# Performance work log

Measured on AMD Instinct MI355X. Metric: run time of the kernel, lower is better.

Reference implementation:

```python
import jax, jax.numpy as jnp
import numpy as np

NEG_INF = -1e6  # d2l masked_softmax fill value


def setup_inputs() -> dict:
    key = jax.random.key(0)
    ks = jax.random.split(key, 7)
    B, Q, K, D, H = 16, 64, 512, 256, 256
    querys = jax.random.normal(ks[0], (B, Q, D), dtype=jnp.float32)
    keys = jax.random.normal(ks[1], (B, K, D), dtype=jnp.float32)
    values = jax.random.normal(ks[2], (B, K, D), dtype=jnp.float32)
    valid_lens = jax.random.randint(ks[3], (B,), 1, K + 1)
    # learned parameters (Linear weights stored as (in, out) for x @ W)
    Wq = jax.random.normal(ks[4], (D, H), dtype=jnp.float32) / np.sqrt(D)
    Wk = jax.random.normal(ks[5], (D, H), dtype=jnp.float32) / np.sqrt(D)
    w_v = jax.random.normal(ks[6], (H,), dtype=jnp.float32) / np.sqrt(H)
    return {"querys": querys, "keys": keys, "values": values,
            "valid_lens": valid_lens, "Wq": Wq, "Wk": Wk, "w_v": w_v}


def reference(querys, keys, values, valid_lens, Wq, Wk, w_v):
    B, Q, _ = querys.shape
    K = keys.shape[1]
    q = querys @ Wq                      # (B, Q, H)
    k = keys @ Wk                        # (B, K, H)
    features = jnp.tanh(q[:, :, None, :] + k[:, None, :, :])   # (B, Q, K, H)
    scores = jnp.einsum('bqkh,h->bqk', features, w_v)           # (B, Q, K)
    # masked softmax over key axis: positions >= valid_len get -1e6
    mask = jnp.arange(K)[None, None, :] < valid_lens[:, None, None]  # (B,1,K)
    scores = jnp.where(mask, scores, NEG_INF)
    attn = jax.nn.softmax(scores, axis=-1)                       # (B, Q, K)
    return jnp.einsum('bqk,bkd->bqd', attn, values)              # (B, Q, D)
```

## Files before the change

### kernel.cpp

```cpp
#include <hip/hip_runtime.h>

#define BB 16
#define QQ 64
#define KK 512
#define DD 256
#define HH 256
#define KTILE 128
#define NZ 4
#define LDST 56

#define LOG2E2 2.88539008177792681f

typedef unsigned int uint;
typedef unsigned short ushort;
typedef __attribute__((ext_vector_type(8))) short bf16x8;
typedef __attribute__((ext_vector_type(8))) unsigned short ushort8;
typedef __attribute__((ext_vector_type(4))) float f32x4;

__device__ __forceinline__ float fast_exp2(float x) {
#if __has_builtin(__builtin_amdgcn_exp2f)
    return __builtin_amdgcn_exp2f(x);
#else
    return exp2f(x);
#endif
}

__device__ __forceinline__ ushort f32_to_bf16_rtne(float x) {
    uint u = __float_as_uint(x);
    u = (u + 0x7FFFu + ((u >> 16) & 1u)) >> 16;
    return (ushort)u;
}

__device__ __forceinline__ void cvt8(uint4 u, float4& a, float4& b) {
    a.x = __uint_as_float(u.x << 16); a.y = __uint_as_float(u.x & 0xFFFF0000u);
    a.z = __uint_as_float(u.y << 16); a.w = __uint_as_float(u.y & 0xFFFF0000u);
    b.x = __uint_as_float(u.z << 16); b.y = __uint_as_float(u.z & 0xFFFF0000u);
    b.z = __uint_as_float(u.w << 16); b.w = __uint_as_float(u.w & 0xFFFF0000u);
}

__global__ __launch_bounds__(256) void proj_both(
        const float* __restrict__ Xq, const float* __restrict__ Wq, float* __restrict__ Yq,
        const float* __restrict__ Xk, const float* __restrict__ Wk, ushort* __restrict__ Yk16,
        const int* __restrict__ valid_lens) {
    __shared__ ushort As[64 * LDST];
    __shared__ ushort Bt[64 * LDST];
    const int rt = blockIdx.x;
    const bool is_q = (rt < 16);
    const float* X; const float* W; int row0;
    if (is_q) { X = Xq; W = Wq; row0 = rt * 64; }
    else {
        X = Xk; W = Wk; row0 = (rt - 16) * 64;
        const int bb    = row0 >> 9;
        const int local = row0 & 511;
        if (local >= valid_lens[bb]) return;
    }
    const int col0 = blockIdx.y * 64;
    const int tid  = threadIdx.x;
    const int lane = tid & 63;
    const int w    = tid >> 6;

    f32x4 acc[4] = {{0.f,0.f,0.f,0.f}, {0.f,0.f,0.f,0.f},
                    {0.f,0.f,0.f,0.f}, {0.f,0.f,0.f,0.f}};

    const int ar = tid >> 2;
    const int ak = (tid & 3) * 8;
    const int bc = tid & 15;
    const int bk = tid >> 4;

    for (int k0 = 0; k0 < HH; k0 += 32) {
        {
            const float* xp = X + (size_t)(row0 + ar) * HH + k0 + ak;
            float4 x0 = *(const float4*)(xp);
            float4 x1 = *(const float4*)(xp + 4);
            ushort8 o;
            o[0] = f32_to_bf16_rtne(x0.x); o[1] = f32_to_bf16_rtne(x0.y);
            o[2] = f32_to_bf16_rtne(x0.z); o[3] = f32_to_bf16_rtne(x0.w);
            o[4] = f32_to_bf16_rtne(x1.x); o[5] = f32_to_bf16_rtne(x1.y);
            o[6] = f32_to_bf16_rtne(x1.z); o[7] = f32_to_bf16_rtne(x1.w);
            *(ushort8*)(&As[ar * LDST + ak]) = o;
        }
        {
            #pragma unroll
            for (int s = 0; s < 2; ++s) {
                float4 wv = *(const float4*)(W + (size_t)(k0 + bk + 16*s) * HH + col0 + bc*4);
                Bt[(bc*4 + 0) * LDST + bk + 16*s] = f32_to_bf16_rtne(wv.x);
                Bt[(bc*4 + 1) * LDST + bk + 16*s] = f32_to_bf16_rtne(wv.y);
                Bt[(bc*4 + 2) * LDST + bk + 16*s] = f32_to_bf16_rtne(wv.z);
                Bt[(bc*4 + 3) * LDST + bk + 16*s] = f32_to_bf16_rtne(wv.w);
            }
        }
        __syncthreads();

        const bf16x8 af = *(const bf16x8*)(&As[(w*16 + (lane & 15)) * LDST + (lane >> 4) * 8]);
        #pragma unroll
        for (int ct = 0; ct < 4; ++ct) {
            const bf16x8 bf = *(const bf16x8*)(&Bt[(ct*16 + (lane & 15)) * LDST + (lane >> 4) * 8]);
            acc[ct] = __builtin_amdgcn_mfma_f32_16x16x32_bf16(af, bf, acc[ct], 0, 0, 0);
        }
        __syncthreads();
    }

    const int orow = row0 + w*16 + (lane >> 4) * 4;
    const int ocol = col0 + (lane & 15);
    if (is_q) {
        #pragma unroll
        for (int ct = 0; ct < 4; ++ct)
            #pragma unroll
            for (int j = 0; j < 4; ++j)
                Yq[(size_t)(orow + j) * HH + ocol + ct*16] = acc[ct][j] * LOG2E2;
    } else {
        #pragma unroll
        for (int ct = 0; ct < 4; ++ct)
            #pragma unroll
            for (int j = 0; j < 4; ++j)
                Yk16[(size_t)(orow + j) * HH + ocol + ct*16] =
                    f32_to_bf16_rtne(acc[ct][j] * LOG2E2);
    }
}

__global__ __launch_bounds__(256) void fused_flash(
        const float* __restrict__ qf, const ushort* __restrict__ kf16,
        const float* __restrict__ w_v, const int* __restrict__ valid_lens,
        const float* __restrict__ values,
        float* __restrict__ pm, float* __restrict__ pl, float* __restrict__ po) {
    __shared__ float qls[8][16][20];
    __shared__ float sc[8][KTILE];
    __shared__ float pp[8][KTILE];
    __shared__ float red[4][8][DD];

    const int tid  = threadIdx.x;
    const int lane = tid & 63;
    const int w    = tid >> 6;
    const int hg   = lane & 15;
    const int ksub = lane >> 4;
    const int h0   = hg * 16;

    int TT = 0;
    #pragma unroll
    for (int i = 0; i < BB; ++i)
        TT += (valid_lens[i] + KTILE - 1) >> 7;

    const int xcd = blockIdx.x & 7;
    const int j   = blockIdx.x >> 3;
    const int tl  = xcd + 8 * (j >> 3);
    const int oct = j & 7;
    if (tl >= TT) return;
    const int q0 = oct * 8;

    int bb = 0, zz = 0, vlb = 1, acc = 0;
    #pragma unroll
    for (int i = 0; i < BB; ++i) {
        const int v   = valid_lens[i];
        const int nzi = (v + KTILE - 1) >> 7;
        const bool hit = (tl >= acc) && (tl < acc + nzi);
        if (hit) { bb = i; zz = tl - acc; vlb = v; }
        acc += nzi;
    }
    const int tile_lo = zz * KTILE;
    const int tile_hi = (tile_lo + KTILE < vlb) ? (tile_lo + KTILE) : vlb;

    float4 nw[4];
    float wvsum = 0.f;
    #pragma unroll
    for (int i = 0; i < 4; ++i) {
        float4 wv4 = *(const float4*)(w_v + h0 + i*4);
        wvsum += ((wv4.x + wv4.y) + (wv4.z + wv4.w));
        nw[i] = make_float4(-2.f*wv4.x, -2.f*wv4.y, -2.f*wv4.z, -2.f*wv4.w);
    }

    {
        const int q = tid >> 5, s = tid & 31;
        const int sh = s >> 1, half = s & 1;
        const float* qp = qf + (size_t)(bb*QQ + q0 + q) * HH + sh*16 + half*8;
        float4 xa = *(const float4*)(qp);
        float4 xb = *(const float4*)(qp + 4);
        *(float4*)(&qls[q][sh][half*8])     = xa;
        *(float4*)(&qls[q][sh][half*8 + 4]) = xb;
    }
    #pragma unroll
    for (int i = 0; i < 4; ++i) {
        const int slot = tid + i*256;
        sc[slot >> 7][slot & 127] = -1e6f;
    }

    const int lo  = tile_lo + w * 32;
    int hi = lo + 32; hi = (hi > tile_hi) ? tile_hi : hi;
    const int cnt = hi - lo;
    const int ng  = (cnt <= 0) ? 0 : ((cnt + 3) >> 2);

    __syncthreads();

    {
        const size_t brows = (size_t)bb * KK;
        uint4 c0, c1;
        if (ng > 0) {
            int row = lo + ksub;
            row = (row < tile_hi) ? row : (tile_hi - 1);
            const ushort* p = kf16 + (brows + row) * HH + h0;
            c0 = *(const uint4*)(p);
            c1 = *(const uint4*)(p + 8);
        }
        for (int g = 0; g < ng; ++g) {
            uint4 n0, n1;
            const bool more = (g + 1 < ng);
            if (more) {
                int row = lo + (g+1)*4 + ksub;
                row = (row < tile_hi) ? row : (tile_hi - 1);
                const ushort* p = kf16 + (brows + row) * HH + h0;
                n0 = *(const uint4*)(p);
                n1 = *(const uint4*)(p + 8);
            }
            float4 kv[4];
            cvt8(c0, kv[0], kv[1]);
            cvt8(c1, kv[2], kv[3]);

            const int k = lo + g*4 + ksub;
            #pragma unroll
            for (int pass = 0; pass < 2; ++pass) {
                float s4[4];
                #pragma unroll
                for (int qi = 0; qi < 4; ++qi) {
                    const int q = pass*4 + qi;
                    float a0 = wvsum, a1 = 0.f, a2 = 0.f, a3 = 0.f;
                    #pragma unroll
                    for (int i = 0; i < 4; ++i) {
                        const float4 qv = *(const float4*)(&qls[q][hg][i*4]);
                        float e0 = fast_exp2(qv.x + kv[i].x);
                        float e1 = fast_exp2(qv.y + kv[i].y);
                        float e2 = fast_exp2(qv.z + kv[i].z);
                        float e3 = fast_exp2(qv.w + kv[i].w);
                        a0 = fmaf(nw[i].x, __builtin_amdgcn_rcpf(e0 + 1.f), a0);
                        a1 = fmaf(nw[i].y, __builtin_amdgcn_rcpf(e1 + 1.f), a1);
                        a2 = fmaf(nw[i].z, __builtin_amdgcn_rcpf(e2 + 1.f), a2);
                        a3 = fmaf(nw[i].w, __builtin_amdgcn_rcpf(e3 + 1.f), a3);
                    }
                    s4[qi] = (a0 + a1) + (a2 + a3);
                }
                #pragma unroll
                for (int off = 8; off; off >>= 1) {
                    #pragma unroll
                    for (int qi = 0; qi < 4; ++qi)
                        s4[qi] += __shfl_xor(s4[qi], off);
                }
                if (hg == 0 && k < hi) {
                    #pragma unroll
                    for (int qi = 0; qi < 4; ++qi)
                        sc[pass*4 + qi][k - tile_lo] = s4[qi];
                }
            }
            if (more) { c0 = n0; c1 = n1; }
        }
    }
    __syncthreads();

    #pragma unroll
    for (int r = 0; r < 2; ++r) {
        const int q = 2*w + r;
        float s0 = sc[q][lane*2], s1 = sc[q][lane*2 + 1];
        float m = fmaxf(s0, s1);
        #pragma unroll
        for (int off = 32; off; off >>= 1) m = fmaxf(m, __shfl_xor(m, off));
        float p0 = __expf(s0 - m), p1 = __expf(s1 - m);
        float l = p0 + p1;
        #pragma unroll
        for (int off = 32; off; off >>= 1) l += __shfl_xor(l, off);
        pp[q][lane*2]     = p0;
        pp[q][lane*2 + 1] = p1;
        if (lane == 0) {
            const int id = ((bb*QQ + q0 + q) << 2) + zz;
            pm[id] = m; pl[id] = l;
        }
    }
    __syncthreads();

    {
        const float* V = values + (size_t)bb * KK * DD + lane*4;
        float4 a0 = make_float4(0.f,0.f,0.f,0.f);
        float4 a1 = a0, a2 = a0, a3 = a0, a4 = a0, a5 = a0, a6 = a0, a7 = a0;
        for (int k = lo; k < hi; ++k) {
            const int kt = k - tile_lo;
            float4 v4 = *(const float4*)(V + (size_t)k * DD);
            const float w0 = pp[0][kt], w1 = pp[1][kt], w2 = pp[2][kt], w3 = pp[3][kt];
            const float w4 = pp[4][kt], w5 = pp[5][kt], w6 = pp[6][kt], w7 = pp[7][kt];
            a0.x = fmaf(w0, v4.x, a0.x); a0.y = fmaf(w0, v4.y, a0.y);
            a0.z = fmaf(w0, v4.z, a0.z); a0.w = fmaf(w0, v4.w, a0.w);
            a1.x = fmaf(w1, v4.x, a1.x); a1.y = fmaf(w1, v4.y, a1.y);
            a1.z = fmaf(w1, v4.z, a1.z); a1.w = fmaf(w1, v4.w, a1.w);
            a2.x = fmaf(w2, v4.x, a2.x); a2.y = fmaf(w2, v4.y, a2.y);
            a2.z = fmaf(w2, v4.z, a2.z); a2.w = fmaf(w2, v4.w, a2.w);
            a3.x = fmaf(w3, v4.x, a3.x); a3.y = fmaf(w3, v4.y, a3.y);
            a3.z = fmaf(w3, v4.z, a3.z); a3.w = fmaf(w3, v4.w, a3.w);
            a4.x = fmaf(w4, v4.x, a4.x); a4.y = fmaf(w4, v4.y, a4.y);
            a4.z = fmaf(w4, v4.z, a4.z); a4.w = fmaf(w4, v4.w, a4.w);
            a5.x = fmaf(w5, v4.x, a5.x); a5.y = fmaf(w5, v4.y, a5.y);
            a5.z = fmaf(w5, v4.z, a5.z); a5.w = fmaf(w5, v4.w, a5.w);
            a6.x = fmaf(w6, v4.x, a6.x); a6.y = fmaf(w6, v4.y, a6.y);
            a6.z = fmaf(w6, v4.z, a6.z); a6.w = fmaf(w6, v4.w, a6.w);
            a7.x = fmaf(w7, v4.x, a7.x); a7.y = fmaf(w7, v4.y, a7.y);
            a7.z = fmaf(w7, v4.z, a7.z); a7.w = fmaf(w7, v4.w, a7.w);
        }
        *(float4*)(&red[w][0][lane*4]) = a0;
        *(float4*)(&red[w][1][lane*4]) = a1;
        *(float4*)(&red[w][2][lane*4]) = a2;
        *(float4*)(&red[w][3][lane*4]) = a3;
        *(float4*)(&red[w][4][lane*4]) = a4;
        *(float4*)(&red[w][5][lane*4]) = a5;
        *(float4*)(&red[w][6][lane*4]) = a6;
        *(float4*)(&red[w][7][lane*4]) = a7;
    }
    __syncthreads();

    #pragma unroll
    for (int i = 0; i < 8; ++i) {
        const int slot = tid + i*256;
        const int q = slot >> 8, d = slot & 255;
        const float o = (red[0][q][d] + red[1][q][d]) + (red[2][q][d] + red[3][q][d]);
        po[(size_t)(((bb*QQ + q0 + q) << 2) + zz) * DD + d] = o;
    }
}

__global__ __launch_bounds__(256) void combine_kernel(
        const float* __restrict__ pm, const float* __restrict__ pl,
        const float* __restrict__ po, const int* __restrict__ valid_lens,
        float* __restrict__ out) {
    const int b   = blockIdx.x;
    const int q   = blockIdx.y;
    const int tid = threadIdx.x;
    const int vl  = valid_lens[b];
    const int nz  = (vl + KTILE - 1) >> 7;
    const int idx4 = (b*QQ + q) << 2;

    float mz[NZ], wz[NZ];
    float M = -3.0e38f;
    #pragma unroll
    for (int z = 0; z < NZ; ++z) {
        mz[z] = (z < nz) ? pm[idx4 + z] : -3.0e38f;
        M = fmaxf(M, mz[z]);
    }
    float L = 0.f;
    #pragma unroll
    for (int z = 0; z < NZ; ++z) {
        wz[z] = (z < nz) ? __expf(mz[z] - M) : 0.f;
        L = fmaf(wz[z], (z < nz) ? pl[idx4 + z] : 0.f, L);
    }
    const float inv = 1.f / L;

    float o = 0.f;
    #pragma unroll
    for (int z = 0; z < NZ; ++z) {
        if (z < nz)
            o = fmaf(wz[z], po[(size_t)(idx4 + z) * DD + tid], o);
    }
    out[(size_t)(b*QQ + q) * DD + tid] = o * inv;
}

extern "C" void kernel_launch(void* const* d_in, const int* in_sizes, int n_in,
                              void* d_out, int out_size, void* d_ws, size_t ws_size,
                              hipStream_t stream) {
    (void)in_sizes; (void)n_in; (void)out_size; (void)ws_size;
    const float* querys     = (const float*)d_in[0];
    const float* keys       = (const float*)d_in[1];
    const float* values     = (const float*)d_in[2];
    const int*   valid_lens = (const int*)d_in[3];
    const float* Wq         = (const float*)d_in[4];
    const float* Wk         = (const float*)d_in[5];
    const float* w_v        = (const float*)d_in[6];
    float* out = (float*)d_out;

    float*  qf    = (float*)d_ws;
    ushort* kfeat = (ushort*)(qf + (size_t)BB*QQ*HH);
    float*  pm    = (float*)(kfeat + (size_t)BB*KK*HH);
    float*  pl    = pm + BB*QQ*NZ;
    float*  po    = pl + BB*QQ*NZ;

    proj_both<<<dim3(16 + BB*KK/64, HH/64), 256, 0, stream>>>(
        querys, Wq, qf, keys, Wk, kfeat, valid_lens);
    fused_flash<<<dim3(2048), 256, 0, stream>>>(
        qf, kfeat, w_v, valid_lens, values, pm, pl, po);
    combine_kernel<<<dim3(BB, QQ), 256, 0, stream>>>(
        pm, pl, po, valid_lens, out);
}
```

Before: 50.96 us.

## Repartition fused_flash into 512-thread blocks covering 4 queries per key tile

Each fused_flash block now handles 4 query rows instead of 8 and uses 8 waves of 16 keys each instead of 4 waves of 32. The grid becomes 1024 blocks of 512 threads with simple linear tile indexing, dropping the XCD-aware swizzle. The intent is shorter per-wave key loops, more waves per block, and lower per-thread register pressure from fewer accumulators. In exchange each key-feature and value tile is reloaded by twice as many blocks, the final reduction sums over 8 waves instead of 4, and only half the waves do softmax work.

After: 54.73 us. +7.4%, slower.

```diff
diff --git a/kernel.cpp b/kernel.cpp
--- a/kernel.cpp
+++ b/kernel.cpp
@@ -118,15 +118,25 @@
     }
 }
 
-__global__ __launch_bounds__(256) void fused_flash(
+__global__ __launch_bounds__(512) void fused_flash(
         const float* __restrict__ qf, const ushort* __restrict__ kf16,
         const float* __restrict__ w_v, const int* __restrict__ valid_lens,
         const float* __restrict__ values,
         float* __restrict__ pm, float* __restrict__ pl, float* __restrict__ po) {
-    __shared__ float qls[8][16][20];
-    __shared__ float sc[8][KTILE];
-    __shared__ float pp[8][KTILE];
-    __shared__ float red[4][8][DD];
+    __shared__ float qls[4][16][20];
+    __shared__ float sc[4][KTILE];
+    __shared__ float pp[4][KTILE];
+    __shared__ float red[8][4][DD];
+
+    int TT = 0;
+    #pragma unroll
+    for (int i = 0; i < BB; ++i)
+        TT += (valid_lens[i] + KTILE - 1) >> 7;
+
+    const int t = blockIdx.x;
+    if (t >= TT * 16) return;
+    const int tile_idx = t >> 4;
+    const int q0       = (t & 15) * 4;
 
     const int tid  = threadIdx.x;
     const int lane = tid & 63;
@@ -135,25 +145,13 @@
     const int ksub = lane >> 4;
     const int h0   = hg * 16;
 
-    int TT = 0;
-    #pragma unroll
-    for (int i = 0; i < BB; ++i)
-        TT += (valid_lens[i] + KTILE - 1) >> 7;
-
-    const int xcd = blockIdx.x & 7;
-    const int j   = blockIdx.x >> 3;
-    const int tl  = xcd + 8 * (j >> 3);
-    const int oct = j & 7;
-    if (tl >= TT) return;
-    const int q0 = oct * 8;
-
     int bb = 0, zz = 0, vlb = 1, acc = 0;
     #pragma unroll
     for (int i = 0; i < BB; ++i) {
         const int v   = valid_lens[i];
         const int nzi = (v + KTILE - 1) >> 7;
-        const bool hit = (tl >= acc) && (tl < acc + nzi);
-        if (hit) { bb = i; zz = tl - acc; vlb = v; }
+        const bool hit = (tile_idx >= acc) && (tile_idx < acc + nzi);
+        if (hit) { bb = i; zz = tile_idx - acc; vlb = v; }
         acc += nzi;
     }
     const int tile_lo = zz * KTILE;
@@ -169,22 +167,16 @@
     }
 
     {
-        const int q = tid >> 5, s = tid & 31;
-        const int sh = s >> 1, half = s & 1;
-        const float* qp = qf + (size_t)(bb*QQ + q0 + q) * HH + sh*16 + half*8;
-        float4 xa = *(const float4*)(qp);
-        float4 xb = *(const float4*)(qp + 4);
-        *(float4*)(&qls[q][sh][half*8])     = xa;
-        *(float4*)(&qls[q][sh][half*8 + 4]) = xb;
-    }
-    #pragma unroll
-    for (int i = 0; i < 4; ++i) {
-        const int slot = tid + i*256;
-        sc[slot >> 7][slot & 127] = -1e6f;
-    }
-
-    const int lo  = tile_lo + w * 32;
-    int hi = lo + 32; hi = (hi > tile_hi) ? tile_hi : hi;
+        const int q = tid >> 7, s = tid & 127;
+        const float* qp = qf + (size_t)(bb*QQ + q0 + q) * HH + s*2;
+        float2 x = *(const float2*)(qp);
+        qls[q][s >> 3][(s & 7) * 2]     = x.x;
+        qls[q][s >> 3][(s & 7) * 2 + 1] = x.y;
+    }
+    sc[tid >> 7][tid & 127] = -1e6f;
+
+    const int lo  = tile_lo + w * 16;
+    int hi = lo + 16; hi = (hi > tile_hi) ? tile_hi : hi;
     const int cnt = hi - lo;
     const int ng  = (cnt <= 0) ? 0 : ((cnt + 3) >> 2);
 
@@ -214,13 +206,12 @@
             cvt8(c0, kv[0], kv[1]);
             cvt8(c1, kv[2], kv[3]);
 
-            const int k = lo + g*4 + ksub;
+            float s4[4];
             #pragma unroll
             for (int pass = 0; pass < 2; ++pass) {
-                float s4[4];
                 #pragma unroll
-                for (int qi = 0; qi < 4; ++qi) {
-                    const int q = pass*4 + qi;
+                for (int qi = 0; qi < 2; ++qi) {
+                    const int q = pass*2 + qi;
                     float a0 = wvsum, a1 = 0.f, a2 = 0.f, a3 = 0.f;
                     #pragma unroll
                     for (int i = 0; i < 4; ++i) {
@@ -234,28 +225,28 @@
                         a2 = fmaf(nw[i].z, __builtin_amdgcn_rcpf(e2 + 1.f), a2);
                         a3 = fmaf(nw[i].w, __builtin_amdgcn_rcpf(e3 + 1.f), a3);
                     }
-                    s4[qi] = (a0 + a1) + (a2 + a3);
+                    s4[pass*2 + qi] = (a0 + a1) + (a2 + a3);
                 }
+            }
+            #pragma unroll
+            for (int off = 8; off; off >>= 1) {
                 #pragma unroll
-                for (int off = 8; off; off >>= 1) {
-                    #pragma unroll
-                    for (int qi = 0; qi < 4; ++qi)
-                        s4[qi] += __shfl_xor(s4[qi], off);
-                }
-                if (hg == 0 && k < hi) {
-                    #pragma unroll
-                    for (int qi = 0; qi < 4; ++qi)
-                        sc[pass*4 + qi][k - tile_lo] = s4[qi];
-                }
+                for (int qi = 0; qi < 4; ++qi)
+                    s4[qi] += __shfl_xor(s4[qi], off);
+            }
+            const int k = lo + g*4 + ksub;
+            if (hg == 0 && k < hi) {
+                #pragma unroll
+                for (int qi = 0; qi < 4; ++qi)
+                    sc[qi][k - tile_lo] = s4[qi];
             }
             if (more) { c0 = n0; c1 = n1; }
         }
     }
     __syncthreads();
 
-    #pragma unroll
-    for (int r = 0; r < 2; ++r) {
-        const int q = 2*w + r;
+    if (w < 4) {
+        const int q = w;
         float s0 = sc[q][lane*2], s1 = sc[q][lane*2 + 1];
         float m = fmaxf(s0, s1);
         #pragma unroll
@@ -276,12 +267,12 @@
     {
         const float* V = values + (size_t)bb * KK * DD + lane*4;
         float4 a0 = make_float4(0.f,0.f,0.f,0.f);
-        float4 a1 = a0, a2 = a0, a3 = a0, a4 = a0, a5 = a0, a6 = a0, a7 = a0;
+        float4 a1 = a0, a2 = a0, a3 = a0;
         for (int k = lo; k < hi; ++k) {
             const int kt = k - tile_lo;
             float4 v4 = *(const float4*)(V + (size_t)k * DD);
-            const float w0 = pp[0][kt], w1 = pp[1][kt], w2 = pp[2][kt], w3 = pp[3][kt];
-            const float w4 = pp[4][kt], w5 = pp[5][kt], w6 = pp[6][kt], w7 = pp[7][kt];
+            const float w0 = pp[0][kt], w1 = pp[1][kt];
+            const float w2 = pp[2][kt], w3 = pp[3][kt];
             a0.x = fmaf(w0, v4.x, a0.x); a0.y = fmaf(w0, v4.y, a0.y);
             a0.z = fmaf(w0, v4.z, a0.z); a0.w = fmaf(w0, v4.w, a0.w);
             a1.x = fmaf(w1, v4.x, a1.x); a1.y = fmaf(w1, v4.y, a1.y);
@@ -290,31 +281,21 @@
             a2.z = fmaf(w2, v4.z, a2.z); a2.w = fmaf(w2, v4.w, a2.w);
             a3.x = fmaf(w3, v4.x, a3.x); a3.y = fmaf(w3, v4.y, a3.y);
             a3.z = fmaf(w3, v4.z, a3.z); a3.w = fmaf(w3, v4.w, a3.w);
-            a4.x = fmaf(w4, v4.x, a4.x); a4.y = fmaf(w4, v4.y, a4.y);
-            a4.z = fmaf(w4, v4.z, a4.z); a4.w = fmaf(w4, v4.w, a4.w);
-            a5.x = fmaf(w5, v4.x, a5.x); a5.y = fmaf(w5, v4.y, a5.y);
-            a5.z = fmaf(w5, v4.z, a5.z); a5.w = fmaf(w5, v4.w, a5.w);
-            a6.x = fmaf(w6, v4.x, a6.x); a6.y = fmaf(w6, v4.y, a6.y);
-            a6.z = fmaf(w6, v4.z, a6.z); a6.w = fmaf(w6, v4.w, a6.w);
-            a7.x = fmaf(w7, v4.x, a7.x); a7.y = fmaf(w7, v4.y, a7.y);
-            a7.z = fmaf(w7, v4.z, a7.z); a7.w = fmaf(w7, v4.w, a7.w);
         }
         *(float4*)(&red[w][0][lane*4]) = a0;
         *(float4*)(&red[w][1][lane*4]) = a1;
         *(float4*)(&red[w][2][lane*4]) = a2;
         *(float4*)(&red[w][3][lane*4]) = a3;
-        *(float4*)(&red[w][4][lane*4]) = a4;
-        *(float4*)(&red[w][5][lane*4]) = a5;
-        *(float4*)(&red[w][6][lane*4]) = a6;
-        *(float4*)(&red[w][7][lane*4]) = a7;
     }
     __syncthreads();
 
     #pragma unroll
-    for (int i = 0; i < 8; ++i) {
-        const int slot = tid + i*256;
+    for (int i = 0; i < 2; ++i) {
+        const int slot = tid + i*512;
         const int q = slot >> 8, d = slot & 255;
-        const float o = (red[0][q][d] + red[1][q][d]) + (red[2][q][d] + red[3][q][d]);
+        float o = 0.f;
+        #pragma unroll
+        for (int ww = 0; ww < 8; ++ww) o += red[ww][q][d];
         po[(size_t)(((bb*QQ + q0 + q) << 2) + zz) * DD + d] = o;
     }
 }
@@ -375,7 +356,7 @@
 
     proj_both<<<dim3(16 + BB*KK/64, HH/64), 256, 0, stream>>>(
         querys, Wq, qf, keys, Wk, kfeat, valid_lens);
-    fused_flash<<<dim3(2048), 256, 0, stream>>>(
+    fused_flash<<<dim3(1024), 512, 0, stream>>>(
         qf, kfeat, w_v, valid_lens, values, pm, pl, po);
     combine_kernel<<<dim3(BB, QQ), 256, 0, stream>>>(
         pm, pl, po, valid_lens, out);
```
